# Kernel optimization log

Hardware: AMD Instinct MI355X
Metric: run time of the kernel (lower is better)

Reference implementation:

```python
import jax, jax.numpy as jnp
import numpy as np
from jax import lax

C = 128; HEADS = 16; HD = 8; EPS = 1e-5

def _conv3x3(x, w):
    return lax.conv_general_dilated(x, w, (1, 1), 'SAME', dimension_numbers=('NCHW', 'OIHW', 'NCHW'))

def _cbr3(x, w, g, b):
    # Conv3x3 + BatchNorm(eval, running stats folded -> per-channel affine) + ReLU
    return jax.nn.relu(_conv3x3(x, w) * g[:, None, None] + b[:, None, None])

def _cbr1(x, w, g, b):
    y = jnp.einsum('bchw,oc->bohw', x, w)
    return jax.nn.relu(y * g[:, None, None] + b[:, None, None])

def _ln(t, g, b):
    mu = t.mean(-1, keepdims=True)
    va = ((t - mu) ** 2).mean(-1, keepdims=True)
    return (t - mu) / jnp.sqrt(va + EPS) * g + b

def _gconv1x1(xf, w, b, groups):
    # grouped 1x1 conv on flattened spatial dim: xf [B,Cin,N], w [Cout, Cin//groups]
    B, Cin, N = xf.shape
    Cout = w.shape[0]
    y = jnp.einsum('bgcn,goc->bgon', xf.reshape(B, groups, Cin // groups, N),
                   w.reshape(groups, Cout // groups, Cin // groups))
    return y.reshape(B, Cout, N) + b[:, None]

def _ss_softmax(a):
    # sign * sqrt(|a| + 1e-5) then softmax (GISSA's custom transform)
    a = jnp.sign(a) * jnp.sqrt(jnp.abs(a) + 1e-5)
    return jax.nn.softmax(a, axis=-1)

def _gissa(ximg, qkv_w, qkv_b, g, b, qkv2_w, qkv2_b):
    B, Cc, H, W = ximg.shape
    N = H * W
    xf = ximg.reshape(B, Cc, N)
    qkv = _gconv1x1(xf, qkv_w, qkv_b, HEADS).reshape(B, 3, HEADS, HD, N)
    q, k, v = qkv[:, 0], qkv[:, 1], qkv[:, 2]
    attn = _ss_softmax(jnp.einsum('bhdn,bhen->bhde', q, k) * HD ** -0.5)  # [B,h,hd,hd]
    x1 = jnp.einsum('bhde,bhen->bhdn', attn, v).reshape(B, Cc, N) + xf
    x1 = x1.reshape(B, HEADS, HD, N).transpose(0, 2, 1, 3).reshape(B, Cc, N)  # channel shuffle
    y = x1 * g[:, None] + b[:, None]  # BatchNorm eval affine
    xr = jax.nn.relu(y)
    qkv2 = _gconv1x1(xr, qkv2_w, qkv2_b, HD).reshape(B, 3, HD, HEADS, N)
    q2, k2, v2 = qkv2[:, 0], qkv2[:, 1], qkv2[:, 2]
    attn2 = _ss_softmax(jnp.einsum('bdhn,bdgn->bdhg', q2, k2) * HEADS ** -0.5)  # [B,hd,h,h]
    o = jnp.einsum('bdhg,bdgn->bdhn', attn2, v2).transpose(0, 2, 1, 3).reshape(B, Cc, N) + y
    return o.reshape(B, Cc, H, W)

def _swsa_calc(ximg, pi_w, pi_b, g, b, po_w, po_b):
    B, Cc, H, W = ximg.shape
    t = jnp.einsum('bcn,oc->bon', ximg.reshape(B, Cc, H * W), pi_w) + pi_b[:, None]
    t = t * g[:, None] + b[:, None]  # BN affine
    q = t[:, :Cc].transpose(0, 2, 1)  # [B,N,C]
    v = t[:, Cc:].transpose(0, 2, 1)
    atn = jax.nn.softmax(jnp.einsum('bnc,bmc->bnm', q, q) * Cc ** -0.5, axis=-1)
    y = jnp.einsum('bnm,bmc->bnc', atn, v).transpose(0, 2, 1)  # [B,C,N]
    y = (jnp.einsum('bcn,oc->bon', y, po_w) + po_b[:, None]).reshape(B, Cc, H, W)
    return y, atn

def _swsa_reuse(ximg, atn, pi_w, pi_b, g, b, po_w, po_b):
    B, Cc, H, W = ximg.shape
    t = jnp.einsum('bcn,oc->bon', ximg.reshape(B, Cc, H * W), pi_w) + pi_b[:, None]
    t = t * g[:, None] + b[:, None]
    v = t.transpose(0, 2, 1)
    y = (jnp.einsum('bnm,bmc->bnc', atn, v) * Cc ** -0.5).transpose(0, 2, 1)
    return (jnp.einsum('bcn,oc->bon', y, po_w) + po_b[:, None]).reshape(B, Cc, H, W)

def _forward(x, ssfe_w, ssfe_g, ssfe_b, cc_w, cc_g, cc_b, ln1_g, ln1_b, qkv_w, qkv_b, gbn_g, gbn_b, qkv2_w, qkv2_b, ln2_g, ln2_b, mlp_w1, mlp_b1, mlp_w2, mlp_b2, cs_w, cs_g, cs_b, lfe0_w, lfe0_g, lfe0_b, s0_pi_w, s0_pi_b, s0_bn_g, s0_bn_b, s0_po_w, s0_po_b, lfe1_w, lfe1_g, lfe1_b, s1_pi_w, s1_pi_b, s1_bn_g, s1_bn_b, s1_po_w, s1_po_b, lamuda, fc_w):
    B, Cin, H, W = x.shape
    N = H * W
    # SSFE stem (approximated as Conv3x3+BN+ReLU; source def unavailable)
    xs = _cbr3(x, ssfe_w, ssfe_g, ssfe_b)
    # channel branch: 1x1 CBR + SIT (LN -> GISSA -> residual -> LN -> MLP -> residual)
    xc = _cbr1(xs, cc_w, cc_g, cc_b)
    t = xc.reshape(B, C, N).transpose(0, 2, 1)  # [B,N,C]
    cur = _ln(t, ln1_g, ln1_b).transpose(0, 2, 1).reshape(B, C, H, W)
    t = t + _gissa(cur, qkv_w, qkv_b, gbn_g, gbn_b, qkv2_w, qkv2_b).reshape(B, C, N).transpose(0, 2, 1)
    h = _ln(t, ln2_g, ln2_b)
    h = jax.nn.gelu(h @ mlp_w1.T + mlp_b1, approximate=False) @ mlp_w2.T + mlp_b2
    t = t + h
    xc = t.transpose(0, 2, 1).reshape(B, C, H, W)
    # spatial branch: 3x3 CBR + SCA (LFE + SWSA with attention reuse)
    xp = _cbr3(xs, cs_w, cs_g, cs_b)
    xp = _cbr3(xp, lfe0_w, lfe0_g, lfe0_b) + xp
    y, atn = _swsa_calc(xp, s0_pi_w, s0_pi_b, s0_bn_g, s0_bn_b, s0_po_w, s0_po_b)
    xp = y + xp
    xp = _cbr3(xp, lfe1_w, lfe1_g, lfe1_b) + xp
    xp = _swsa_reuse(xp, atn, s1_pi_w, s1_pi_b, s1_bn_g, s1_bn_b, s1_po_w, s1_po_b) + xp
    lmd = jax.nn.sigmoid(lamuda[0])
    out = lmd * xc + (1.0 - lmd) * xp
    return out.mean(axis=(2, 3)) @ fc_w.T  # global avg pool + fc (dropout p=0 for HUST2013)

def setup_inputs():
    ks = iter(jax.random.split(jax.random.key(0), 64))
    def rn(shape, scale=0.05):
        return jax.random.normal(next(ks), shape, jnp.float32) * scale
    ones = lambda *s: jnp.ones(s, jnp.float32)
    zeros = lambda *s: jnp.zeros(s, jnp.float32)
    return dict(
        x=jax.random.normal(next(ks), (32, 144, 32, 32), jnp.float32),
        ssfe_w=rn((144, 144, 3, 3)), ssfe_g=ones(144), ssfe_b=zeros(144),
        cc_w=rn((128, 144)), cc_g=ones(128), cc_b=zeros(128),
        ln1_g=ones(128), ln1_b=zeros(128),
        qkv_w=rn((384, 8)), qkv_b=zeros(384),
        gbn_g=ones(128), gbn_b=zeros(128),
        qkv2_w=rn((384, 16)), qkv2_b=zeros(384),
        ln2_g=ones(128), ln2_b=zeros(128),
        mlp_w1=rn((512, 128)), mlp_b1=zeros(512),
        mlp_w2=rn((128, 512)), mlp_b2=zeros(128),
        cs_w=rn((128, 144, 3, 3)), cs_g=ones(128), cs_b=zeros(128),
        lfe0_w=rn((128, 128, 3, 3)), lfe0_g=ones(128), lfe0_b=zeros(128),
        s0_pi_w=rn((256, 128)), s0_pi_b=zeros(256), s0_bn_g=ones(256), s0_bn_b=zeros(256),
        s0_po_w=rn((128, 128)), s0_po_b=zeros(128),
        lfe1_w=rn((128, 128, 3, 3)), lfe1_g=ones(128), lfe1_b=zeros(128),
        s1_pi_w=rn((128, 128)), s1_pi_b=zeros(128), s1_bn_g=ones(128), s1_bn_b=zeros(128),
        s1_po_w=rn((128, 128)), s1_po_b=zeros(128),
        lamuda=jnp.full((1,), 0.5, jnp.float32),
        fc_w=rn((16, 128)),
    )

def reference(x, ssfe_w, ssfe_g, ssfe_b, cc_w, cc_g, cc_b, ln1_g, ln1_b, qkv_w, qkv_b, gbn_g, gbn_b, qkv2_w, qkv2_b, ln2_g, ln2_b, mlp_w1, mlp_b1, mlp_w2, mlp_b2, cs_w, cs_g, cs_b, lfe0_w, lfe0_g, lfe0_b, s0_pi_w, s0_pi_b, s0_bn_g, s0_bn_b, s0_po_w, s0_po_b, lfe1_w, lfe1_g, lfe1_b, s1_pi_w, s1_pi_b, s1_bn_g, s1_bn_b, s1_po_w, s1_po_b, lamuda, fc_w):
    return _forward(x, ssfe_w, ssfe_g, ssfe_b, cc_w, cc_g, cc_b, ln1_g, ln1_b, qkv_w, qkv_b, gbn_g, gbn_b, qkv2_w, qkv2_b, ln2_g, ln2_b, mlp_w1, mlp_b1, mlp_w2, mlp_b2, cs_w, cs_g, cs_b, lfe0_w, lfe0_g, lfe0_b, s0_pi_w, s0_pi_b, s0_bn_g, s0_bn_b, s0_po_w, s0_po_b, lfe1_w, lfe1_g, lfe1_b, s1_pi_w, s1_pi_b, s1_bn_g, s1_bn_b, s1_po_w, s1_po_b, lamuda, fc_w)
```

## Files before the change

kernel.cpp:

```cpp
#include <hip/hip_runtime.h>
#include <math.h>


static constexpr int NPIX = 1024;

typedef __attribute__((ext_vector_type(8))) short bf16x8;
typedef __attribute__((ext_vector_type(4))) float f32x4;
typedef __attribute__((ext_vector_type(8))) unsigned short u16x8;
typedef __attribute__((ext_vector_type(4))) unsigned short u16x4;

static __device__ __forceinline__ unsigned short f2bf(float f) {
    unsigned u = __builtin_bit_cast(unsigned, f);
    unsigned r = (u + 0x7fffu + ((u >> 16) & 1u)) >> 16;
    return (unsigned short)r;
}
static __device__ __forceinline__ float bf2f(unsigned short u) {
    unsigned v = ((unsigned)u) << 16;
    return __builtin_bit_cast(float, v);
}

__global__ __launch_bounds__(256) void prepack_convs(
    const float* __restrict__ ssfe_w, const float* __restrict__ cs_w,
    const float* __restrict__ lfe0_w, const float* __restrict__ lfe1_w,
    unsigned short* __restrict__ wssfe, unsigned short* __restrict__ wcs,
    unsigned short* __restrict__ wlfe0, unsigned short* __restrict__ wlfe1)
{
    int idx = blockIdx.x * 256 + threadIdx.x;
    const float* src;
    unsigned short* dst;
    int k, Cout, CIN, CINP;
    if (idx < 207360) {
        src = ssfe_w; dst = wssfe; k = idx; Cout = 144; CIN = 144; CINP = 160;
    } else if (idx < 391680) {
        src = cs_w; dst = wcs; k = idx - 207360; Cout = 128; CIN = 144; CINP = 160;
    } else if (idx < 539136) {
        src = lfe0_w; dst = wlfe0; k = idx - 391680; Cout = 128; CIN = 128; CINP = 128;
    } else if (idx < 686592) {
        src = lfe1_w; dst = wlfe1; k = idx - 539136; Cout = 128; CIN = 128; CINP = 128;
    } else return;
    int ci = k % CINP;
    int rem = k / CINP;
    int co = rem % Cout;
    int tap = rem / Cout;
    float v = (ci < CIN) ? src[((size_t)co * CIN + ci) * 9 + tap] : 0.f;
    dst[k] = f2bf(v);
}

__global__ __launch_bounds__(256) void prepack_lins(
    const float* __restrict__ cc_w, const float* __restrict__ pi0_w,
    const float* __restrict__ pi1_w, const float* __restrict__ po0_w,
    const float* __restrict__ po1_w, const float* __restrict__ w1,
    const float* __restrict__ w2, unsigned short* __restrict__ o)
{
    int idx = blockIdx.x * 256 + threadIdx.x;
    if (idx >= 233472) return;
    float v;
    if (idx < 20480) {
        int ci = idx % 160, co = idx / 160;
        v = (ci < 144) ? cc_w[co * 144 + ci] : 0.f;
    } else if (idx < 53248) {
        v = pi0_w[idx - 20480];
    } else if (idx < 69632) {
        v = pi1_w[idx - 53248];
    } else if (idx < 86016) {
        v = po0_w[idx - 69632];
    } else if (idx < 102400) {
        v = po1_w[idx - 86016];
    } else if (idx < 167936) {
        v = w1[idx - 102400];
    } else {
        v = w2[idx - 167936];
    }
    o[idx] = f2bf(v);
}

__global__ __launch_bounds__(256) void cvt_xT_kernel(
    const float* __restrict__ x, unsigned short* __restrict__ xT0)
{
    __shared__ unsigned short T[64 * 168];
    const int tid = threadIdx.x;
    const int b = blockIdx.x;
    const int px0 = blockIdx.y << 6;
    const float* xb = x + ((size_t)b * 144 << 10) + px0;

#pragma unroll 1
    for (int idx = tid; idx < 72 * 64; idx += 256) {
        const int c2 = idx >> 6, px = idx & 63;
        float a = xb[((size_t)(2 * c2) << 10) + px];
        float c = xb[((size_t)(2 * c2 + 1) << 10) + px];
        *(unsigned*)&T[px * 168 + 2 * c2] =
            (unsigned)f2bf(a) | ((unsigned)f2bf(c) << 16);
    }
#pragma unroll 1
    for (int idx = tid; idx < 64 * 8; idx += 256) {
        const int px = idx >> 3, pr = idx & 7;
        *(unsigned*)&T[px * 168 + 144 + pr * 2] = 0u;
    }
    __syncthreads();

#pragma unroll 1
    for (int idx = tid; idx < 64 * 20; idx += 256) {
        const int px = idx / 20;
        const int chunk = idx - px * 20;
        *(u16x8*)(xT0 + ((size_t)((b << 10) + px0 + px)) * 160 + chunk * 8) =
            *(const u16x8*)&T[px * 168 + chunk * 8];
    }
}

__global__ __launch_bounds__(256) void conv3x3_ssfe_kernel(
    const unsigned short* __restrict__ xT,
    const unsigned short* __restrict__ wrep,
    const float* __restrict__ g, const float* __restrict__ bb,
    unsigned short* __restrict__ outT)
{
    constexpr int CINP = 160, PITCH = 168, NCHK = 20;
    __shared__ unsigned short X[130 * PITCH];
    const int tid = threadIdx.x;
    const int b = blockIdx.x, gr = blockIdx.y;
    const int pbase = gr << 6;
    const int gbase = pbase - 33;
    const int wid = tid >> 6, lane = tid & 63;
    const int ll = lane & 15, lq = lane >> 4;
    const unsigned short* xb = xT + ((size_t)b << 10) * CINP;

#pragma unroll 1
    for (int idx = tid; idx < 130 * NCHK; idx += 256) {
        const int row = idx / NCHK;
        const int chunk = idx - row * NCHK;
        const int gp = gbase + row;
        u16x8 v = {};
        if (gp >= 0 && gp < 1024)
            v = *(const u16x8*)(xb + (size_t)gp * CINP + chunk * 8);
        *(u16x8*)&X[row * PITCH + chunk * 8] = v;
    }
    __syncthreads();

    if (wid == 3) {
#pragma unroll
        for (int j = 0; j < 4; ++j) {
            const int px = pbase + j * 16 + ll;
            u16x4 z = {};
            *(u16x4*)(outT + ((size_t)((b << 10) + px)) * 160 + 144 + lq * 4) = z;
        }
        return;
    }

    const int co0w = wid * 48;
    f32x4 acc[3][4];
#pragma unroll
    for (int i = 0; i < 3; ++i)
#pragma unroll
        for (int j = 0; j < 4; ++j)
#pragma unroll
            for (int r = 0; r < 4; ++r) acc[i][j][r] = 0.f;

#pragma unroll
    for (int tap = 0; tap < 9; ++tap) {
        const int soff = (tap / 3) * 32 + (tap % 3);
        const int dx = tap % 3;
#pragma unroll
        for (int kc = 0; kc < CINP / 32; ++kc) {
            bf16x8 bfv[4];
#pragma unroll
            for (int j = 0; j < 4; ++j) {
                const int p = j * 16 + ll;
                bf16x8 v = *(const bf16x8*)&X[(p + soff) * PITCH + kc * 32 + lq * 8];
                const bool zed = (dx == 0 && (j & 1) == 0 && ll == 0) ||
                                 (dx == 2 && (j & 1) == 1 && ll == 15);
                if (zed) { bf16x8 z = {}; v = z; }
                bfv[j] = v;
            }
            const unsigned short* wb =
                wrep + ((size_t)tap * 144 + co0w) * CINP + kc * 32 + lq * 8;
#pragma unroll
            for (int i = 0; i < 3; ++i) {
                bf16x8 af = *(const bf16x8*)(wb + (size_t)(i * 16 + ll) * CINP);
#pragma unroll
                for (int j = 0; j < 4; ++j)
                    acc[i][j] = __builtin_amdgcn_mfma_f32_16x16x32_bf16(
                        af, bfv[j], acc[i][j], 0, 0, 0);
            }
        }
    }

#pragma unroll
    for (int i = 0; i < 3; ++i) {
        const int cob = co0w + i * 16 + lq * 4;
        float gv[4], bv[4];
#pragma unroll
        for (int r = 0; r < 4; ++r) { gv[r] = g[cob + r]; bv[r] = bb[cob + r]; }
#pragma unroll
        for (int j = 0; j < 4; ++j) {
            const int px = pbase + j * 16 + ll;
            u16x4 tp;
#pragma unroll
            for (int r = 0; r < 4; ++r)
                tp[r] = f2bf(fmaxf(acc[i][j][r] * gv[r] + bv[r], 0.f));
            *(u16x4*)(outT + ((size_t)((b << 10) + px)) * 160 + cob) = tp;
        }
    }
}

template <int CINP>
__global__ __launch_bounds__(256) void conv3x3_lds_kernel(
    const unsigned short* __restrict__ xT,
    const unsigned short* __restrict__ wrep,
    const float* __restrict__ g, const float* __restrict__ bb,
    const unsigned short* __restrict__ resT,
    unsigned short* __restrict__ outT, int Cout)
{
    constexpr int PITCH = CINP + 8;
    constexpr int NCHK = CINP / 8;
    __shared__ unsigned short X[130 * PITCH];
    const int tid = threadIdx.x;
    const int b = blockIdx.x, gr = blockIdx.y;
    const int pbase = gr << 6;
    const int gbase = pbase - 33;
    const int wid = tid >> 6, lane = tid & 63;
    const int ll = lane & 15, lq = lane >> 4;
    const int co0w = wid << 5;
    const unsigned short* xb = xT + ((size_t)b << 10) * CINP;

#pragma unroll 1
    for (int idx = tid; idx < 130 * NCHK; idx += 256) {
        const int row = idx / NCHK;
        const int chunk = idx - row * NCHK;
        const int gp = gbase + row;
        u16x8 v = {};
        if (gp >= 0 && gp < 1024)
            v = *(const u16x8*)(xb + (size_t)gp * CINP + chunk * 8);
        *(u16x8*)&X[row * PITCH + chunk * 8] = v;
    }
    __syncthreads();

    f32x4 acc[2][4];
#pragma unroll
    for (int i = 0; i < 2; ++i)
#pragma unroll
        for (int j = 0; j < 4; ++j)
#pragma unroll
            for (int r = 0; r < 4; ++r) acc[i][j][r] = 0.f;

#pragma unroll
    for (int tap = 0; tap < 9; ++tap) {
        const int soff = (tap / 3) * 32 + (tap % 3);
        const int dx = tap % 3;
#pragma unroll
        for (int kc = 0; kc < CINP / 32; ++kc) {
            bf16x8 bfv[4];
#pragma unroll
            for (int j = 0; j < 4; ++j) {
                const int p = j * 16 + ll;
                bf16x8 v = *(const bf16x8*)&X[(p + soff) * PITCH + kc * 32 + lq * 8];
                const bool zed = (dx == 0 && (j & 1) == 0 && ll == 0) ||
                                 (dx == 2 && (j & 1) == 1 && ll == 15);
                if (zed) { bf16x8 z = {}; v = z; }
                bfv[j] = v;
            }
            const unsigned short* wb =
                wrep + ((size_t)tap * Cout + co0w) * CINP + kc * 32 + lq * 8;
#pragma unroll
            for (int i = 0; i < 2; ++i) {
                bf16x8 af = *(const bf16x8*)(wb + (size_t)(i * 16 + ll) * CINP);
#pragma unroll
                for (int j = 0; j < 4; ++j)
                    acc[i][j] = __builtin_amdgcn_mfma_f32_16x16x32_bf16(
                        af, bfv[j], acc[i][j], 0, 0, 0);
            }
        }
    }

#pragma unroll
    for (int i = 0; i < 2; ++i) {
        const int cob = co0w + i * 16 + lq * 4;
        float gv[4], bv[4];
#pragma unroll
        for (int r = 0; r < 4; ++r) { gv[r] = g[cob + r]; bv[r] = bb[cob + r]; }
#pragma unroll
        for (int j = 0; j < 4; ++j) {
            const int px = pbase + j * 16 + ll;
            const size_t rowT = ((size_t)((b << 10) + px)) << 7;
            u16x4 rv = {};
            if (resT) rv = *(const u16x4*)(resT + rowT + cob);
            u16x4 tp;
#pragma unroll
            for (int r = 0; r < 4; ++r) {
                float v = fmaxf(acc[i][j][r] * gv[r] + bv[r], 0.f);
                if (resT) v += bf2f(rv[r]);
                tp[r] = f2bf(v);
            }
            *(u16x4*)(outT + rowT + cob) = tp;
        }
    }
}

template <int KP>
__global__ __launch_bounds__(256) void lin_mfma_kernel(
    const unsigned short* __restrict__ xT, const unsigned short* __restrict__ wbf,
    const float* __restrict__ bias0, const float* __restrict__ g,
    const float* __restrict__ bb, const unsigned short* __restrict__ resT,
    float* __restrict__ outF, unsigned short* __restrict__ outBF,
    unsigned short* __restrict__ outT, int do_relu)
{
    const int tid = threadIdx.x;
    const int b = blockIdx.x;
    const int n0 = blockIdx.y << 6;
    const int wid = tid >> 6, lane = tid & 63;
    const int ll = lane & 15, lq = lane >> 4;
    const unsigned short* xb = xT + (size_t)((b << 10) + n0) * KP;

    f32x4 acc[2][4];
#pragma unroll
    for (int i = 0; i < 2; ++i)
#pragma unroll
        for (int j = 0; j < 4; ++j)
#pragma unroll
            for (int r = 0; r < 4; ++r) acc[i][j][r] = 0.f;

#pragma unroll
    for (int kk = 0; kk < KP / 32; ++kk) {
        bf16x8 af[2], bfv[4];
#pragma unroll
        for (int i = 0; i < 2; ++i)
            af[i] = *(const bf16x8*)(wbf + (size_t)(wid * 32 + i * 16 + ll) * KP + kk * 32 + lq * 8);
#pragma unroll
        for (int j = 0; j < 4; ++j)
            bfv[j] = *(const bf16x8*)(xb + (size_t)(j * 16 + ll) * KP + kk * 32 + lq * 8);
#pragma unroll
        for (int i = 0; i < 2; ++i)
#pragma unroll
            for (int j = 0; j < 4; ++j)
                acc[i][j] = __builtin_amdgcn_mfma_f32_16x16x32_bf16(af[i], bfv[j], acc[i][j], 0, 0, 0);
    }

#pragma unroll
    for (int i = 0; i < 2; ++i) {
        const int cob = wid * 32 + i * 16 + lq * 4;
        float b0v[4], gv[4], bv[4];
#pragma unroll
        for (int r = 0; r < 4; ++r) {
            b0v[r] = bias0 ? bias0[cob + r] : 0.f;
            gv[r] = g ? g[cob + r] : 1.f;
            bv[r] = g ? bb[cob + r] : 0.f;
        }
#pragma unroll
        for (int j = 0; j < 4; ++j) {
            const int px = n0 + j * 16 + ll;
            const size_t rowT = ((size_t)((b << 10) + px)) << 7;
            u16x4 rv = {};
            if (resT) rv = *(const u16x4*)(resT + rowT + cob);
            u16x4 tp;
#pragma unroll
            for (int r = 0; r < 4; ++r) {
                const int co = cob + r;
                float v = acc[i][j][r] + b0v[r];
                v = v * gv[r] + bv[r];
                if (do_relu) v = fmaxf(v, 0.f);
                if (resT) v += bf2f(rv[r]);
                if (outF) outF[((size_t)((b << 7) + co) << 10) + px] = v;
                unsigned short h = f2bf(v);
                if (outBF) outBF[((size_t)((b << 7) + co) << 10) + px] = h;
                tp[r] = h;
            }
            if (outT) *(u16x4*)(outT + rowT + cob) = tp;
        }
    }
}

__global__ __launch_bounds__(256) void ln_kernel(
    const float* __restrict__ in, const float* __restrict__ g,
    const float* __restrict__ bb, unsigned short* __restrict__ out_bf,
    unsigned short* __restrict__ outT)
{
    const int tid = threadIdx.x;
    const int b = blockIdx.x >> 2;
    const int n = ((blockIdx.x & 3) << 8) + tid;
    const float* ib = in + ((size_t)b << 17) + n;
    float s = 0.f, sq = 0.f;
#pragma unroll 8
    for (int c = 0; c < 128; ++c) {
        float v = ib[(size_t)c << 10];
        s += v;
        sq += v * v;
    }
    const float mu = s * 0.0078125f;
    const float r = rsqrtf(sq * 0.0078125f - mu * mu + 1e-5f);
    unsigned short* obf = out_bf + ((size_t)b << 17) + n;
    unsigned short* oT = outT + (((size_t)b << 10) + n) * 128;
#pragma unroll 2
    for (int c0 = 0; c0 < 128; c0 += 8) {
        u16x8 pk;
#pragma unroll
        for (int e = 0; e < 8; ++e) {
            const int c = c0 + e;
            float v = ib[(size_t)c << 10];
            float y = (v - mu) * r * g[c] + bb[c];
            unsigned short h = f2bf(y);
            obf[(size_t)c << 10] = h;
            pk[e] = h;
        }
        *(u16x8*)(oT + c0) = pk;
    }
}

__global__ __launch_bounds__(256) void gram_kernel(
    const unsigned short* __restrict__ Xbf, float* __restrict__ G)
{
    __shared__ unsigned short Xs[128 * 128];
    const int tid = threadIdx.x;
    const int b = blockIdx.x >> 2;
    const int rg = blockIdx.x & 3;
    const int wid = tid >> 6, lane = tid & 63;
    const int lq = lane >> 4, ll = lane & 15;
    const unsigned short* Xb = Xbf + ((size_t)b << 17);

    f32x4 acc[2][2];
#pragma unroll
    for (int mi = 0; mi < 2; ++mi)
#pragma unroll
        for (int ci = 0; ci < 2; ++ci)
#pragma unroll
            for (int r = 0; r < 4; ++r) acc[mi][ci][r] = 0.f;

#pragma unroll 1
    for (int nt = 0; nt < 8; ++nt) {
        const int n0 = nt << 7;
#pragma unroll
        for (int p = 0; p < 8; ++p) {
            const int ch = (p << 4) + (tid >> 4);
            const int seg = (tid & 15) << 3;
            *(u16x8*)&Xs[ch * 128 + (seg ^ ((ch & 7) << 3))] =
                *(const u16x8*)(Xb + ((size_t)ch << 10) + n0 + seg);
        }
        __syncthreads();
#pragma unroll
        for (int ks = 0; ks < 4; ++ks) {
            bf16x8 af[2], bf_[2];
#pragma unroll
            for (int mi = 0; mi < 2; ++mi) {
                const int ar = (rg << 5) + mi * 16 + ll;
                af[mi] = *(const bf16x8*)&Xs[ar * 128 + ((ks * 32 + lq * 8) ^ ((ar & 7) << 3))];
            }
#pragma unroll
            for (int ci = 0; ci < 2; ++ci) {
                const int br = (wid << 5) + ci * 16 + ll;
                bf_[ci] = *(const bf16x8*)&Xs[br * 128 + ((ks * 32 + lq * 8) ^ ((br & 7) << 3))];
            }
#pragma unroll
            for (int mi = 0; mi < 2; ++mi)
#pragma unroll
                for (int ci = 0; ci < 2; ++ci)
                    acc[mi][ci] = __builtin_amdgcn_mfma_f32_16x16x32_bf16(
                        af[mi], bf_[ci], acc[mi][ci], 0, 0, 0);
        }
        __syncthreads();
    }
    float* Gb = G + ((size_t)b << 14);
#pragma unroll
    for (int mi = 0; mi < 2; ++mi)
#pragma unroll
        for (int ci = 0; ci < 2; ++ci)
#pragma unroll
            for (int r = 0; r < 4; ++r) {
                const int row = (rg << 5) + mi * 16 + lq * 4 + r;
                const int col = (wid << 5) + ci * 16 + ll;
                Gb[row * 128 + col] = acc[mi][ci][r];
            }
}

__global__ __launch_bounds__(256) void sums_kernel(
    const unsigned short* __restrict__ Xbf, float* __restrict__ S)
{
    const int tid = threadIdx.x;
    const int b = blockIdx.x;
    const int ch = tid >> 1, half = tid & 1;
    const unsigned short* p = Xbf + ((size_t)b << 17) + ((size_t)ch << 10) + half * 512;
    float s = 0.f;
#pragma unroll 4
    for (int i = 0; i < 64; ++i) {
        u16x8 v = *(const u16x8*)(p + i * 8);
#pragma unroll
        for (int e = 0; e < 8; ++e) s += bf2f(v[e]);
    }
    s += __shfl_xor(s, 1);
    if (half == 0) S[(b << 7) + ch] = s;
}

__global__ __launch_bounds__(64) void mats1_kernel(
    const float* __restrict__ G, const float* __restrict__ S,
    const float* __restrict__ qkv_w, const float* __restrict__ qkv_b,
    const float* __restrict__ g, const float* __restrict__ bb,
    unsigned short* __restrict__ M1, float* __restrict__ c1)
{
    const int lane = threadIdx.x;
    const int b = blockIdx.x >> 4, h = blockIdx.x & 15;
    const float* Gb = G + ((size_t)b << 14);
    const float* Sb = S + (b << 7);
    const int d = lane >> 3, e = lane & 7;
    const int qch = h * 8 + d, kch = 128 + h * 8 + e;
    const int qoff = (qch / 24) * 8, koff = (kch / 24) * 8;
    float wq[8], wk[8];
#pragma unroll
    for (int i = 0; i < 8; ++i) {
        wq[i] = qkv_w[qch * 8 + i];
        wk[i] = qkv_w[kch * 8 + i];
    }
    float s = 0.f;
#pragma unroll
    for (int i = 0; i < 8; ++i) {
        float gu = 0.f;
#pragma unroll
        for (int j = 0; j < 8; ++j) gu += Gb[(qoff + i) * 128 + koff + j] * wk[j];
        s += wq[i] * gu;
    }
    const float bq = qkv_b[qch], bk = qkv_b[kch];
    float swk = 0.f, swq = 0.f;
#pragma unroll
    for (int j = 0; j < 8; ++j) { swk += wk[j] * Sb[koff + j]; swq += wq[j] * Sb[qoff + j]; }
    s += bq * swk + bk * swq + 1024.f * bq * bk;
    s *= 0.35355339059327373f;
    float a = (s > 0.f) ? sqrtf(s + 1e-5f) : ((s < 0.f) ? -sqrtf(1e-5f - s) : 0.f);
    float mx = a;
    mx = fmaxf(mx, __shfl_xor(mx, 1));
    mx = fmaxf(mx, __shfl_xor(mx, 2));
    mx = fmaxf(mx, __shfl_xor(mx, 4));
    float p = __expf(a - mx);
    float den = p;
    den += __shfl_xor(den, 1);
    den += __shfl_xor(den, 2);
    den += __shfl_xor(den, 4);
    const float A = p / den;

    const int l = e;
    const int cp = d * 16 + h;
    float row[16];
#pragma unroll
    for (int j = 0; j < 16; ++j) row[j] = 0.f;
    float cacc = 0.f;
#pragma unroll
    for (int e2 = 0; e2 < 8; ++e2) {
        const float Ae = __shfl(A, d * 8 + e2);
        const int vch = 256 + h * 8 + e2;
        const int voff = (vch / 24) * 8;
        cacc += Ae * qkv_b[vch];
        if ((voff >> 4) == l) {
            const int base = voff & 15;
#pragma unroll
            for (int j = 0; j < 8; ++j) row[base + j] += Ae * qkv_w[vch * 8 + j];
        }
    }
    const int idc = h * 8 + d;
    if ((idc >> 4) == l) row[idc & 15] += 1.f;
    const float gg = g[cp];
    unsigned short* mrow = M1 + ((size_t)b << 14) + cp * 128 + l * 16;
#pragma unroll
    for (int j = 0; j < 16; ++j) mrow[j] = f2bf(gg * row[j]);
    if (l == 0) c1[(b << 7) + cp] = gg * cacc + bb[cp];
}

__global__ __launch_bounds__(256) void mats2_kernel(
    const float* __restrict__ G, const float* __restrict__ S,
    const float* __restrict__ qkv2_w, const float* __restrict__ qkv2_b,
    unsigned short* __restrict__ M2, float* __restrict__ c2)
{
    const int tid = threadIdx.x;
    const int b = blockIdx.x >> 3, d = blockIdx.x & 7;
    const float* Gb = G + ((size_t)b << 14);
    const float* Sb = S + (b << 7);
    const int h = tid >> 4, gq = tid & 15;
    const int q2ch = d * 16 + h, k2ch = 128 + d * 16 + gq;
    const int qoff = (q2ch / 48) * 16, koff = (k2ch / 48) * 16;
    float wq[16], wk[16];
#pragma unroll
    for (int i = 0; i < 16; ++i) {
        wq[i] = qkv2_w[q2ch * 16 + i];
        wk[i] = qkv2_w[k2ch * 16 + i];
    }
    float s = 0.f;
#pragma unroll
    for (int i = 0; i < 16; ++i) {
        float gu = 0.f;
#pragma unroll
        for (int j = 0; j < 16; ++j) gu += Gb[(qoff + i) * 128 + koff + j] * wk[j];
        s += wq[i] * gu;
    }
    const float bq = qkv2_b[q2ch], bk = qkv2_b[k2ch];
    float swk = 0.f, swq = 0.f;
#pragma unroll
    for (int j = 0; j < 16; ++j) { swk += wk[j] * Sb[koff + j]; swq += wq[j] * Sb[qoff + j]; }
    s += bq * swk + bk * swq + 1024.f * bq * bk;
    s *= 0.25f;
    float a = (s > 0.f) ? sqrtf(s + 1e-5f) : ((s < 0.f) ? -sqrtf(1e-5f - s) : 0.f);
    float mx = a;
    mx = fmaxf(mx, __shfl_xor(mx, 1));
    mx = fmaxf(mx, __shfl_xor(mx, 2));
    mx = fmaxf(mx, __shfl_xor(mx, 4));
    mx = fmaxf(mx, __shfl_xor(mx, 8));
    float p = __expf(a - mx);
    float den = p;
    den += __shfl_xor(den, 1);
    den += __shfl_xor(den, 2);
    den += __shfl_xor(den, 4);
    den += __shfl_xor(den, 8);
    const float A2 = p / den;

    const int l = gq;
    float row[8];
#pragma unroll
    for (int j = 0; j < 8; ++j) row[j] = 0.f;
    float cacc = 0.f;
#pragma unroll
    for (int g2 = 0; g2 < 16; ++g2) {
        const float Ag = __shfl(A2, (tid & 48) + g2);
        const int v2ch = 256 + d * 16 + g2;
        const int voff = (v2ch / 48) * 16;
        cacc += Ag * qkv2_b[v2ch];
        if ((l >> 1) == (voff >> 4)) {
            const int base = (l & 1) * 8;
#pragma unroll
            for (int j = 0; j < 8; ++j) row[j] += Ag * qkv2_w[v2ch * 16 + base + j];
        }
    }
    const int c = h * 8 + d;
    unsigned short* mrow = M2 + ((size_t)b << 14) + c * 128 + l * 8;
#pragma unroll
    for (int j = 0; j < 8; ++j) mrow[j] = f2bf(row[j]);
    if (l == 0) c2[(b << 7) + c] = cacc;
}

__global__ __launch_bounds__(256) void apply1_mfma_kernel(
    const unsigned short* __restrict__ curT, const unsigned short* __restrict__ M1bf,
    const float* __restrict__ c1, float* __restrict__ ybuf,
    unsigned short* __restrict__ yrbf, unsigned short* __restrict__ yrT)
{
    const int tid = threadIdx.x;
    const int b = blockIdx.x >> 3;
    const int n0 = (blockIdx.x & 7) << 7;
    const int wid = tid >> 6, lane = tid & 63;
    const int wr = wid >> 1, wc = wid & 1;
    const int ll = lane & 15, lq = lane >> 4;
    const unsigned short* Mb = M1bf + ((size_t)b << 14);
    const unsigned short* xb = curT + (((size_t)b << 10) + n0 + wc * 64) * 128;

    f32x4 acc[4][4];
#pragma unroll
    for (int i = 0; i < 4; ++i)
#pragma unroll
        for (int j = 0; j < 4; ++j)
#pragma unroll
            for (int r = 0; r < 4; ++r) acc[i][j][r] = 0.f;

#pragma unroll
    for (int kk = 0; kk < 4; ++kk) {
        bf16x8 af[4], bfv[4];
#pragma unroll
        for (int i = 0; i < 4; ++i)
            af[i] = *(const bf16x8*)(Mb + (size_t)(wr * 64 + i * 16 + ll) * 128 + kk * 32 + lq * 8);
#pragma unroll
        for (int j = 0; j < 4; ++j)
            bfv[j] = *(const bf16x8*)(xb + (size_t)(j * 16 + ll) * 128 + kk * 32 + lq * 8);
#pragma unroll
        for (int i = 0; i < 4; ++i)
#pragma unroll
            for (int j = 0; j < 4; ++j)
                acc[i][j] = __builtin_amdgcn_mfma_f32_16x16x32_bf16(af[i], bfv[j], acc[i][j], 0, 0, 0);
    }

#pragma unroll
    for (int i = 0; i < 4; ++i) {
        const int cob = wr * 64 + i * 16 + lq * 4;
        float c1v[4];
#pragma unroll
        for (int r = 0; r < 4; ++r) c1v[r] = c1[(b << 7) + cob + r];
#pragma unroll
        for (int j = 0; j < 4; ++j) {
            const int px = n0 + wc * 64 + j * 16 + ll;
            u16x4 tp;
#pragma unroll
            for (int r = 0; r < 4; ++r) {
                const int co = cob + r;
                const float v = acc[i][j][r] + c1v[r];
                const size_t oi = ((size_t)(b * 128 + co) << 10) + px;
                ybuf[oi] = v;
                const unsigned short h = f2bf(fmaxf(v, 0.f));
                yrbf[oi] = h;
                tp[r] = h;
            }
            *(u16x4*)(yrT + (((size_t)b << 10) + px) * 128 + cob) = tp;
        }
    }
}

__global__ __launch_bounds__(256) void apply2_mfma_kernel(
    const unsigned short* __restrict__ yrT, const unsigned short* __restrict__ M2bf,
    const float* __restrict__ c2, const float* __restrict__ ybuf,
    float* __restrict__ t)
{
    const int tid = threadIdx.x;
    const int b = blockIdx.x >> 3;
    const int n0 = (blockIdx.x & 7) << 7;
    const int wid = tid >> 6, lane = tid & 63;
    const int wr = wid >> 1, wc = wid & 1;
    const int ll = lane & 15, lq = lane >> 4;
    const unsigned short* Mb = M2bf + ((size_t)b << 14);
    const unsigned short* xb = yrT + (((size_t)b << 10) + n0 + wc * 64) * 128;

    f32x4 acc[4][4];
#pragma unroll
    for (int i = 0; i < 4; ++i)
#pragma unroll
        for (int j = 0; j < 4; ++j)
#pragma unroll
            for (int r = 0; r < 4; ++r) acc[i][j][r] = 0.f;

#pragma unroll
    for (int kk = 0; kk < 4; ++kk) {
        bf16x8 af[4], bfv[4];
#pragma unroll
        for (int i = 0; i < 4; ++i)
            af[i] = *(const bf16x8*)(Mb + (size_t)(wr * 64 + i * 16 + ll) * 128 + kk * 32 + lq * 8);
#pragma unroll
        for (int j = 0; j < 4; ++j)
            bfv[j] = *(const bf16x8*)(xb + (size_t)(j * 16 + ll) * 128 + kk * 32 + lq * 8);
#pragma unroll
        for (int i = 0; i < 4; ++i)
#pragma unroll
            for (int j = 0; j < 4; ++j)
                acc[i][j] = __builtin_amdgcn_mfma_f32_16x16x32_bf16(af[i], bfv[j], acc[i][j], 0, 0, 0);
    }

#pragma unroll
    for (int i = 0; i < 4; ++i) {
        const int cob = wr * 64 + i * 16 + lq * 4;
        float c2v[4];
#pragma unroll
        for (int r = 0; r < 4; ++r) c2v[r] = c2[(b << 7) + cob + r];
#pragma unroll
        for (int j = 0; j < 4; ++j) {
            const int px = n0 + wc * 64 + j * 16 + ll;
#pragma unroll
            for (int r = 0; r < 4; ++r) {
                const size_t oi = ((size_t)(b * 128 + cob + r) << 10) + px;
                t[oi] += acc[i][j][r] + c2v[r] + ybuf[oi];
            }
        }
    }
}

__global__ __launch_bounds__(256) void mlp_mfma_kernel(
    float* __restrict__ t, const float* __restrict__ ln_g,
    const float* __restrict__ ln_b, const unsigned short* __restrict__ w1bf,
    const float* __restrict__ b1, const unsigned short* __restrict__ w2bf,
    const float* __restrict__ b2)
{
    __shared__ unsigned char lds[16384 + 65536];
    unsigned char* xnb = lds;
    unsigned char* hb = lds + 16384;

    const int tid = threadIdx.x;
    const int b = blockIdx.x >> 4;
    const int n0 = (blockIdx.x & 15) << 6;
    float* tb = t + ((size_t)b << 17) + n0;

    {
        const int px = tid >> 2, q = tid & 3;
        float v[32];
        float s = 0.f, sq = 0.f;
#pragma unroll
        for (int k = 0; k < 32; ++k) {
            float x = tb[((size_t)(q * 32 + k) << 10) + px];
            v[k] = x;
            s += x;
            sq += x * x;
        }
        s += __shfl_xor(s, 1); s += __shfl_xor(s, 2);
        sq += __shfl_xor(sq, 1); sq += __shfl_xor(sq, 2);
        const float mu = s * 0.0078125f;
        const float rstd = rsqrtf(sq * 0.0078125f - mu * mu + 1e-5f);
        const int sw = (px & 7) << 4;
#pragma unroll
        for (int cc = 0; cc < 4; ++cc) {
            u16x8 pk;
#pragma unroll
            for (int e = 0; e < 8; ++e) {
                int c = q * 32 + cc * 8 + e;
                float xv = (v[cc * 8 + e] - mu) * rstd * ln_g[c] + ln_b[c];
                pk[e] = f2bf(xv);
            }
            *(u16x8*)(xnb + px * 256 + ((q * 64 + cc * 16) ^ sw)) = pk;
        }
    }
    __syncthreads();

    const int wid = tid >> 6, lane = tid & 63;
    const int lr = lane & 15, lk = lane >> 4;

#pragma unroll 1
    for (int pass = 0; pass < 2; ++pass) {
        const int hidbase = (wid << 7) + (pass << 6);
        f32x4 acc[4][4];
#pragma unroll
        for (int i = 0; i < 4; ++i)
#pragma unroll
            for (int j = 0; j < 4; ++j)
#pragma unroll
                for (int r = 0; r < 4; ++r) acc[i][j][r] = 0.f;
#pragma unroll
        for (int kk = 0; kk < 4; ++kk) {
            bf16x8 af[4], bfr[4];
#pragma unroll
            for (int i = 0; i < 4; ++i)
                af[i] = *(const bf16x8*)(w1bf + (size_t)(hidbase + i * 16 + lr) * 128 + kk * 32 + lk * 8);
#pragma unroll
            for (int j = 0; j < 4; ++j) {
                const int px = j * 16 + lr;
                bfr[j] = *(const bf16x8*)(xnb + px * 256 + ((kk * 64 + lk * 16) ^ ((px & 7) << 4)));
            }
#pragma unroll
            for (int i = 0; i < 4; ++i)
#pragma unroll
                for (int j = 0; j < 4; ++j)
                    acc[i][j] = __builtin_amdgcn_mfma_f32_16x16x32_bf16(af[i], bfr[j], acc[i][j], 0, 0, 0);
        }
#pragma unroll
        for (int i = 0; i < 4; ++i) {
            const int hid0 = hidbase + i * 16 + lk * 4;
            float bi[4];
#pragma unroll
            for (int r = 0; r < 4; ++r) bi[r] = b1[hid0 + r];
#pragma unroll
            for (int j = 0; j < 4; ++j) {
                const int px = j * 16 + lr;
                u16x4 pk;
#pragma unroll
                for (int r = 0; r < 4; ++r) {
                    float x = acc[i][j][r] + bi[r];
                    float u = 1.5957691f * x * (1.f + 0.044715f * x * x);
                    float gv = x / (1.f + __expf(-u));
                    pk[r] = f2bf(gv);
                }
                *(u16x4*)(hb + px * 1024 + ((hid0 * 2) ^ ((px & 7) << 4))) = pk;
            }
        }
    }
    __syncthreads();

    f32x4 acc2[2][4];
#pragma unroll
    for (int i = 0; i < 2; ++i)
#pragma unroll
        for (int j = 0; j < 4; ++j)
#pragma unroll
            for (int r = 0; r < 4; ++r) acc2[i][j][r] = 0.f;
#pragma unroll 2
    for (int ks = 0; ks < 16; ++ks) {
        bf16x8 af[2], bfr[4];
#pragma unroll
        for (int i = 0; i < 2; ++i)
            af[i] = *(const bf16x8*)(w2bf + (size_t)((wid << 5) + i * 16 + lr) * 512 + ks * 32 + lk * 8);
#pragma unroll
        for (int j = 0; j < 4; ++j) {
            const int px = j * 16 + lr;
            bfr[j] = *(const bf16x8*)(hb + px * 1024 + ((ks * 64 + lk * 16) ^ ((px & 7) << 4)));
        }
#pragma unroll
        for (int i = 0; i < 2; ++i)
#pragma unroll
            for (int j = 0; j < 4; ++j)
                acc2[i][j] = __builtin_amdgcn_mfma_f32_16x16x32_bf16(af[i], bfr[j], acc2[i][j], 0, 0, 0);
    }
#pragma unroll
    for (int i = 0; i < 2; ++i) {
        const int cb = (wid << 5) + i * 16 + lk * 4;
        float b2v[4];
#pragma unroll
        for (int r = 0; r < 4; ++r) b2v[r] = b2[cb + r];
#pragma unroll
        for (int j = 0; j < 4; ++j) {
            const int px = j * 16 + lr;
#pragma unroll
            for (int r = 0; r < 4; ++r) {
                const size_t off = ((size_t)(cb + r) << 10) + px;
                tb[off] += acc2[i][j][r] + b2v[r];
            }
        }
    }
}

__global__ __launch_bounds__(256) void swsa_mfma_kernel(
    const unsigned short* __restrict__ qT, const unsigned short* __restrict__ vbf,
    float* __restrict__ outp, unsigned short* __restrict__ outT, float fscale)
{
    __shared__ unsigned short K_lds[128 * 128];
    __shared__ unsigned short V_lds[128 * 128];
    const int tid = threadIdx.x;
    const int b = blockIdx.x & 31;
    const int n0 = (blockIdx.x >> 5) << 6;
    const int wid = tid >> 6, lane = tid & 63;
    const int lq = lane >> 4, ll = lane & 15;
    const unsigned short* qTb = qT + ((size_t)b << 17);
    const unsigned short* vb = vbf + ((size_t)b << 17);

    bf16x8 aq[4];
    {
        const int row = n0 + wid * 16 + ll;
#pragma unroll
        for (int kk = 0; kk < 4; ++kk)
            aq[kk] = *(const bf16x8*)(qTb + ((size_t)row << 7) + kk * 32 + lq * 8);
    }

    float mrun[4], lrun[4];
#pragma unroll
    for (int i = 0; i < 4; ++i) { mrun[i] = -INFINITY; lrun[i] = 0.f; }
    f32x4 yacc[8];
#pragma unroll
    for (int cj = 0; cj < 8; ++cj)
#pragma unroll
        for (int r = 0; r < 4; ++r) yacc[cj][r] = 0.f;

#pragma unroll 1
    for (int mt = 0; mt < 8; ++mt) {
        const int m0 = mt << 7;
        for (int ch = tid; ch < 2048; ch += 256) {
            const int rr = ch >> 4, e0 = (ch & 15) << 3;
            const int sw = (rr & 7) << 3;
            *(u16x8*)&K_lds[rr * 128 + (e0 ^ sw)] =
                *(const u16x8*)(qTb + ((size_t)(m0 + rr) << 7) + e0);
            *(u16x8*)&V_lds[rr * 128 + (e0 ^ sw)] =
                *(const u16x8*)(vb + ((size_t)rr << 10) + m0 + e0);
        }
        __syncthreads();

        f32x4 sacc[8];
#pragma unroll
        for (int j = 0; j < 8; ++j)
#pragma unroll
            for (int r = 0; r < 4; ++r) sacc[j][r] = 0.f;
#pragma unroll
        for (int j = 0; j < 8; ++j) {
            const int ml = j * 16 + ll;
            const int swk = (ml & 7) << 3;
#pragma unroll
            for (int kk = 0; kk < 4; ++kk) {
                bf16x8 bk = *(const bf16x8*)&K_lds[ml * 128 + ((kk * 32 + lq * 8) ^ swk)];
                sacc[j] = __builtin_amdgcn_mfma_f32_16x16x32_bf16(aq[kk], bk, sacc[j], 0, 0, 0);
            }
        }
        __syncthreads();

        float pmax[4];
#pragma unroll
        for (int i = 0; i < 4; ++i) pmax[i] = -INFINITY;
#pragma unroll
        for (int j = 0; j < 8; ++j)
#pragma unroll
            for (int r = 0; r < 4; ++r) {
                float s = sacc[j][r] * 0.08838834764831845f;
                sacc[j][r] = s;
                pmax[r] = fmaxf(pmax[r], s);
            }
        float alpha[4];
#pragma unroll
        for (int i = 0; i < 4; ++i) {
            float m = pmax[i];
            m = fmaxf(m, __shfl_xor(m, 1));
            m = fmaxf(m, __shfl_xor(m, 2));
            m = fmaxf(m, __shfl_xor(m, 4));
            m = fmaxf(m, __shfl_xor(m, 8));
            const float mn = fmaxf(mrun[i], m);
            alpha[i] = __expf(mrun[i] - mn);
            mrun[i] = mn;
        }
        float psum[4];
#pragma unroll
        for (int r = 0; r < 4; ++r) {
            const int nbw = wid * 16 + lq * 4 + r;
            const int sw4 = ((nbw >> 2) & 3) << 4;
            const float mn = mrun[r];
            float ps = 0.f;
#pragma unroll
            for (int j = 0; j < 8; ++j) {
                float p = __expf(sacc[j][r] - mn);
                ps += p;
                K_lds[nbw * 128 + ((j * 16 + ll) ^ sw4)] = f2bf(p);
            }
            psum[r] = ps;
        }
#pragma unroll
        for (int i = 0; i < 4; ++i) {
            float s = psum[i];
            s += __shfl_xor(s, 1);
            s += __shfl_xor(s, 2);
            s += __shfl_xor(s, 4);
            s += __shfl_xor(s, 8);
            lrun[i] = lrun[i] * alpha[i] + s;
        }
#pragma unroll
        for (int cj = 0; cj < 8; ++cj)
#pragma unroll
            for (int r = 0; r < 4; ++r) yacc[cj][r] *= alpha[r];

        bf16x8 ap[4];
        {
            const int nb = wid * 16 + ll;
            const int sw4 = ((nb >> 2) & 3) << 4;
#pragma unroll
            for (int mk = 0; mk < 4; ++mk)
                ap[mk] = *(const bf16x8*)&K_lds[nb * 128 + ((mk * 32 + lq * 8) ^ sw4)];
        }
#pragma unroll
        for (int cj = 0; cj < 8; ++cj) {
            const int cl = cj * 16 + ll;
            const int sw = (cl & 7) << 3;
#pragma unroll
            for (int mk = 0; mk < 4; ++mk) {
                bf16x8 bv = *(const bf16x8*)&V_lds[cl * 128 + ((mk * 32 + lq * 8) ^ sw)];
                yacc[cj] = __builtin_amdgcn_mfma_f32_16x16x32_bf16(ap[mk], bv, yacc[cj], 0, 0, 0);
            }
        }
        __syncthreads();
    }

    const int nbase = n0 + wid * 16 + lq * 4;
    float inv[4];
#pragma unroll
    for (int r = 0; r < 4; ++r) inv[r] = fscale / lrun[r];
#pragma unroll
    for (int cj = 0; cj < 8; ++cj) {
        const int c = cj * 16 + ll;
        float4 o;
        o.x = yacc[cj][0] * inv[0];
        o.y = yacc[cj][1] * inv[1];
        o.z = yacc[cj][2] * inv[2];
        o.w = yacc[cj][3] * inv[3];
        if (outp)
            *(float4*)(outp + ((size_t)(b * 128 + c) << 10) + nbase) = o;
        if (outT) {
            unsigned short* tb = outT + ((size_t)((b << 10) + nbase)) * 128 + c;
            tb[0] = f2bf(o.x);
            tb[128] = f2bf(o.y);
            tb[256] = f2bf(o.z);
            tb[384] = f2bf(o.w);
        }
    }
}

__global__ __launch_bounds__(256) void mean_kernel(
    const float* __restrict__ xc, const float* __restrict__ xp,
    const float* __restrict__ lamuda, float* __restrict__ meanb)
{
    const int wid = threadIdx.x >> 6, lane = threadIdx.x & 63;
    const int row = (blockIdx.x << 2) + wid;
    const float lmd = 1.f / (1.f + __expf(-lamuda[0]));
    const float* a = xc + ((size_t)row << 10) + (lane << 2);
    const float* d = xp + ((size_t)row << 10) + (lane << 2);
    float s = 0.f;
#pragma unroll
    for (int i = 0; i < 4; ++i) {
        float4 va = *(const float4*)(a + (i << 8));
        float4 vd = *(const float4*)(d + (i << 8));
        s += lmd * (va.x + va.y + va.z + va.w) +
             (1.f - lmd) * (vd.x + vd.y + vd.z + vd.w);
    }
#pragma unroll
    for (int o = 1; o < 64; o <<= 1) s += __shfl_xor(s, o);
    if (lane == 0) meanb[row] = s * (1.f / 1024.f);
}

__global__ __launch_bounds__(256) void fc_kernel(
    const float* __restrict__ meanb, const float* __restrict__ fc_w,
    float* __restrict__ outp)
{
    const int idx = blockIdx.x * 256 + threadIdx.x;
    if (idx >= 512) return;
    const int b = idx >> 4, o = idx & 15;
    float s = 0.f;
#pragma unroll 4
    for (int c = 0; c < 128; ++c) s += fc_w[o * 128 + c] * meanb[b * 128 + c];
    outp[b * 16 + o] = s;
}

extern "C" void kernel_launch(void* const* d_in, const int* in_sizes, int n_in,
                              void* d_out, int out_size, void* d_ws, size_t ws_size,
                              hipStream_t stream)
{
    (void)in_sizes; (void)n_in; (void)out_size; (void)ws_size;

    const float* x       = (const float*)d_in[0];
    const float* ssfe_w  = (const float*)d_in[1];
    const float* ssfe_g  = (const float*)d_in[2];
    const float* ssfe_b  = (const float*)d_in[3];
    const float* cc_w    = (const float*)d_in[4];
    const float* cc_g    = (const float*)d_in[5];
    const float* cc_b    = (const float*)d_in[6];
    const float* ln1_g   = (const float*)d_in[7];
    const float* ln1_b   = (const float*)d_in[8];
    const float* qkv_w   = (const float*)d_in[9];
    const float* qkv_b   = (const float*)d_in[10];
    const float* gbn_g   = (const float*)d_in[11];
    const float* gbn_b   = (const float*)d_in[12];
    const float* qkv2_w  = (const float*)d_in[13];
    const float* qkv2_b  = (const float*)d_in[14];
    const float* ln2_g   = (const float*)d_in[15];
    const float* ln2_b   = (const float*)d_in[16];
    const float* mlp_w1  = (const float*)d_in[17];
    const float* mlp_b1  = (const float*)d_in[18];
    const float* mlp_w2  = (const float*)d_in[19];
    const float* mlp_b2  = (const float*)d_in[20];
    const float* cs_w    = (const float*)d_in[21];
    const float* cs_g    = (const float*)d_in[22];
    const float* cs_b    = (const float*)d_in[23];
    const float* lfe0_w  = (const float*)d_in[24];
    const float* lfe0_g  = (const float*)d_in[25];
    const float* lfe0_b  = (const float*)d_in[26];
    const float* s0_pi_w = (const float*)d_in[27];
    const float* s0_pi_b = (const float*)d_in[28];
    const float* s0_bn_g = (const float*)d_in[29];
    const float* s0_bn_b = (const float*)d_in[30];
    const float* s0_po_w = (const float*)d_in[31];
    const float* s0_po_b = (const float*)d_in[32];
    const float* lfe1_w  = (const float*)d_in[33];
    const float* lfe1_g  = (const float*)d_in[34];
    const float* lfe1_b  = (const float*)d_in[35];
    const float* s1_pi_w = (const float*)d_in[36];
    const float* s1_pi_b = (const float*)d_in[37];
    const float* s1_bn_g = (const float*)d_in[38];
    const float* s1_bn_b = (const float*)d_in[39];
    const float* s1_po_w = (const float*)d_in[40];
    const float* s1_po_b = (const float*)d_in[41];
    const float* lamuda  = (const float*)d_in[42];
    const float* fc_w    = (const float*)d_in[43];
    float* out = (float*)d_out;
    float* ws = (float*)d_ws;

    float* xs = ws;
    float* t  = ws + 4718592;
    float* P1 = ws + 8912896;
    float* Qr = ws + 13107200;
    float* P2 = ws + 25690112;
    float* P3 = ws + 29884416;
    (void)P1;

    unsigned short* xT0 = (unsigned short*)Qr;

    unsigned short* curbf = (unsigned short*)Qr;
    unsigned short* curT  = (unsigned short*)(Qr + 2097152);
    unsigned short* yrbf  = (unsigned short*)(Qr + 4194304);
    unsigned short* yrT   = (unsigned short*)(Qr + 6291456);
    unsigned short* xsT   = (unsigned short*)(Qr + 8388608);
    float* ybuf = P2;

    unsigned short* xpT   = (unsigned short*)Qr;
    unsigned short* qT0   = (unsigned short*)Qr;
    unsigned short* v0    = (unsigned short*)(Qr + 2097152);
    unsigned short* yvT   = (unsigned short*)(Qr + 4194304);
    unsigned short* v1    = (unsigned short*)(Qr + 4194304);
    unsigned short* xp3T  = (unsigned short*)(Qr + 6291456);
    unsigned short* yv2T  = (unsigned short*)(Qr + 6291456);
    unsigned short* xp2T  = (unsigned short*)(Qr + 8388608);
    unsigned short* xp4T  = (unsigned short*)(Qr + 8388608);

    unsigned short* linw  = (unsigned short*)(Qr + 11010048);
    unsigned short* wcc   = linw;
    unsigned short* wpi0  = linw + 20480;
    unsigned short* wpi1  = linw + 53248;
    unsigned short* wpo0  = linw + 69632;
    unsigned short* wpo1  = linw + 86016;
    unsigned short* w1bf  = linw + 102400;
    unsigned short* w2bf  = linw + 167936;
    float* meanb = Qr + 11200000;

    float* Gbuf  = P3 + 1048576;
    float* Sbuf  = P3 + 1572864;
    unsigned short* M1bf = (unsigned short*)(P3 + 1576960);
    float* c1buf = P3 + 1839104;
    unsigned short* M2bf = (unsigned short*)(P3 + 1843200);
    float* c2buf = P3 + 2105344;

    unsigned short* wssfe = (unsigned short*)P3;
    unsigned short* wcs   = (unsigned short*)(P3 + 131072);
    unsigned short* wlfe0 = (unsigned short*)(P3 + 262144);
    unsigned short* wlfe1 = (unsigned short*)xs;

    const dim3 blk(256);

    prepack_convs<<<dim3((686592 + 255) / 256), blk, 0, stream>>>(
        ssfe_w, cs_w, lfe0_w, lfe1_w, wssfe, wcs, wlfe0, wlfe1);
    prepack_lins<<<dim3((233472 + 255) / 256), blk, 0, stream>>>(
        cc_w, s0_pi_w, s1_pi_w, s0_po_w, s1_po_w, mlp_w1, mlp_w2, linw);

    cvt_xT_kernel<<<dim3(32, 16), blk, 0, stream>>>(x, xT0);
    conv3x3_ssfe_kernel<<<dim3(32, 16), blk, 0, stream>>>(
        xT0, wssfe, ssfe_g, ssfe_b, xsT);
    lin_mfma_kernel<160><<<dim3(32, 16), blk, 0, stream>>>(
        xsT, wcc, nullptr, cc_g, cc_b, nullptr, t, nullptr, nullptr, 1);

    ln_kernel<<<dim3(128), blk, 0, stream>>>(t, ln1_g, ln1_b, curbf, curT);
    gram_kernel<<<dim3(128), blk, 0, stream>>>(curbf, Gbuf);
    sums_kernel<<<dim3(32), blk, 0, stream>>>(curbf, Sbuf);
    mats1_kernel<<<dim3(512), dim3(64), 0, stream>>>(Gbuf, Sbuf, qkv_w, qkv_b, gbn_g, gbn_b, M1bf, c1buf);
    apply1_mfma_kernel<<<dim3(256), blk, 0, stream>>>(curT, M1bf, c1buf, ybuf, yrbf, yrT);
    gram_kernel<<<dim3(128), blk, 0, stream>>>(yrbf, Gbuf);
    sums_kernel<<<dim3(32), blk, 0, stream>>>(yrbf, Sbuf);
    mats2_kernel<<<dim3(256), blk, 0, stream>>>(Gbuf, Sbuf, qkv2_w, qkv2_b, M2bf, c2buf);
    apply2_mfma_kernel<<<dim3(256), blk, 0, stream>>>(yrT, M2bf, c2buf, ybuf, t);

    mlp_mfma_kernel<<<dim3(512), blk, 0, stream>>>(t, ln2_g, ln2_b, w1bf, mlp_b1, w2bf, mlp_b2);

    conv3x3_lds_kernel<160><<<dim3(32, 16), blk, 0, stream>>>(
        xsT, wcs, cs_g, cs_b, nullptr, xpT, 128);
    conv3x3_lds_kernel<128><<<dim3(32, 16), blk, 0, stream>>>(
        xpT, wlfe0, lfe0_g, lfe0_b, xpT, xp2T, 128);
    lin_mfma_kernel<128><<<dim3(32, 16), blk, 0, stream>>>(
        xp2T, wpi0, s0_pi_b, s0_bn_g, s0_bn_b, nullptr, nullptr, nullptr, qT0, 0);
    lin_mfma_kernel<128><<<dim3(32, 16), blk, 0, stream>>>(
        xp2T, wpi0 + (size_t)128 * 128, s0_pi_b + 128, s0_bn_g + 128, s0_bn_b + 128,
        nullptr, nullptr, v0, nullptr, 0);
    swsa_mfma_kernel<<<dim3(512), blk, 0, stream>>>(qT0, v0, nullptr, yvT, 1.0f);
    lin_mfma_kernel<128><<<dim3(32, 16), blk, 0, stream>>>(
        yvT, wpo0, s0_po_b, nullptr, nullptr, xp2T, nullptr, nullptr, xp3T, 0);
    conv3x3_lds_kernel<128><<<dim3(32, 16), blk, 0, stream>>>(
        xp3T, wlfe1, lfe1_g, lfe1_b, xp3T, xp4T, 128);
    lin_mfma_kernel<128><<<dim3(32, 16), blk, 0, stream>>>(
        xp4T, wpi1, s1_pi_b, s1_bn_g, s1_bn_b, nullptr, nullptr, v1, nullptr, 0);
    swsa_mfma_kernel<<<dim3(512), blk, 0, stream>>>(qT0, v1, nullptr, yv2T, 0.08838834764831845f);
    lin_mfma_kernel<128><<<dim3(32, 16), blk, 0, stream>>>(
        yv2T, wpo1, s1_po_b, nullptr, nullptr, xp4T, P3, nullptr, nullptr, 0);

    mean_kernel<<<dim3(1024), blk, 0, stream>>>(t, P3, lamuda, meanb);
    fc_kernel<<<dim3(2), blk, 0, stream>>>(meanb, fc_w, out);
}
```

Before: 449.4 us.

## Read K/V directly from global in SWSA attention, shrink LDS to per-wave P

The SWSA flash-attention kernel no longer stages 128x128 K and V tiles in shared memory each iteration. It reads MFMA operands straight from global memory and keeps only a small per-wave LDS buffer for the softmax probabilities. This removes the block-wide barriers and cuts LDS use from 64KB to 16KB, which should allow more resident blocks. In exchange, every wave re-reads K and V from global/L2, so the block's K/V loads become redundant across its four waves. The unused fp32 output path is also dropped.

```diff
diff --git a/kernel.cpp b/kernel.cpp
--- a/kernel.cpp
+++ b/kernel.cpp
@@ -889,10 +889,9 @@
 
 __global__ __launch_bounds__(256) void swsa_mfma_kernel(
     const unsigned short* __restrict__ qT, const unsigned short* __restrict__ vbf,
-    float* __restrict__ outp, unsigned short* __restrict__ outT, float fscale)
-{
-    __shared__ unsigned short K_lds[128 * 128];
-    __shared__ unsigned short V_lds[128 * 128];
+    unsigned short* __restrict__ outT, float fscale)
+{
+    __shared__ unsigned short P_lds[4 * 16 * 128];
     const int tid = threadIdx.x;
     const int b = blockIdx.x & 31;
     const int n0 = (blockIdx.x >> 5) << 6;
@@ -900,6 +899,7 @@
     const int lq = lane >> 4, ll = lane & 15;
     const unsigned short* qTb = qT + ((size_t)b << 17);
     const unsigned short* vb = vbf + ((size_t)b << 17);
+    unsigned short* Pw = &P_lds[wid * 16 * 128];
 
     bf16x8 aq[4];
     {
@@ -921,15 +921,6 @@
 #pragma unroll 1
     for (int mt = 0; mt < 8; ++mt) {
         const int m0 = mt << 7;
-        for (int ch = tid; ch < 2048; ch += 256) {
-            const int rr = ch >> 4, e0 = (ch & 15) << 3;
-            const int sw = (rr & 7) << 3;
-            *(u16x8*)&K_lds[rr * 128 + (e0 ^ sw)] =
-                *(const u16x8*)(qTb + ((size_t)(m0 + rr) << 7) + e0);
-            *(u16x8*)&V_lds[rr * 128 + (e0 ^ sw)] =
-                *(const u16x8*)(vb + ((size_t)rr << 10) + m0 + e0);
-        }
-        __syncthreads();
 
         f32x4 sacc[8];
 #pragma unroll
@@ -938,15 +929,13 @@
             for (int r = 0; r < 4; ++r) sacc[j][r] = 0.f;
 #pragma unroll
         for (int j = 0; j < 8; ++j) {
-            const int ml = j * 16 + ll;
-            const int swk = (ml & 7) << 3;
+            const int ml = m0 + j * 16 + ll;
 #pragma unroll
             for (int kk = 0; kk < 4; ++kk) {
-                bf16x8 bk = *(const bf16x8*)&K_lds[ml * 128 + ((kk * 32 + lq * 8) ^ swk)];
+                bf16x8 bk = *(const bf16x8*)(qTb + ((size_t)ml << 7) + kk * 32 + lq * 8);
                 sacc[j] = __builtin_amdgcn_mfma_f32_16x16x32_bf16(aq[kk], bk, sacc[j], 0, 0, 0);
             }
         }
-        __syncthreads();
 
         float pmax[4];
 #pragma unroll
@@ -974,15 +963,15 @@
         float psum[4];
 #pragma unroll
         for (int r = 0; r < 4; ++r) {
-            const int nbw = wid * 16 + lq * 4 + r;
-            const int sw4 = ((nbw >> 2) & 3) << 4;
+            const int rw = lq * 4 + r;
+            const int sw4 = ((rw >> 2) & 3) << 4;
             const float mn = mrun[r];
             float ps = 0.f;
 #pragma unroll
             for (int j = 0; j < 8; ++j) {
                 float p = __expf(sacc[j][r] - mn);
                 ps += p;
-                K_lds[nbw * 128 + ((j * 16 + ll) ^ sw4)] = f2bf(p);
+                Pw[rw * 128 + ((j * 16 + ll) ^ sw4)] = f2bf(p);
             }
             psum[r] = ps;
         }
@@ -1002,23 +991,20 @@
 
         bf16x8 ap[4];
         {
-            const int nb = wid * 16 + ll;
-            const int sw4 = ((nb >> 2) & 3) << 4;
+            const int sw4 = ((ll >> 2) & 3) << 4;
 #pragma unroll
             for (int mk = 0; mk < 4; ++mk)
-                ap[mk] = *(const bf16x8*)&K_lds[nb * 128 + ((mk * 32 + lq * 8) ^ sw4)];
+                ap[mk] = *(const bf16x8*)&Pw[ll * 128 + ((mk * 32 + lq * 8) ^ sw4)];
         }
 #pragma unroll
         for (int cj = 0; cj < 8; ++cj) {
-            const int cl = cj * 16 + ll;
-            const int sw = (cl & 7) << 3;
+            const int c = cj * 16 + ll;
 #pragma unroll
             for (int mk = 0; mk < 4; ++mk) {
-                bf16x8 bv = *(const bf16x8*)&V_lds[cl * 128 + ((mk * 32 + lq * 8) ^ sw)];
+                bf16x8 bv = *(const bf16x8*)(vb + ((size_t)c << 10) + m0 + mk * 32 + lq * 8);
                 yacc[cj] = __builtin_amdgcn_mfma_f32_16x16x32_bf16(ap[mk], bv, yacc[cj], 0, 0, 0);
             }
         }
-        __syncthreads();
     }
 
     const int nbase = n0 + wid * 16 + lq * 4;
@@ -1028,20 +1014,11 @@
 #pragma unroll
     for (int cj = 0; cj < 8; ++cj) {
         const int c = cj * 16 + ll;
-        float4 o;
-        o.x = yacc[cj][0] * inv[0];
-        o.y = yacc[cj][1] * inv[1];
-        o.z = yacc[cj][2] * inv[2];
-        o.w = yacc[cj][3] * inv[3];
-        if (outp)
-            *(float4*)(outp + ((size_t)(b * 128 + c) << 10) + nbase) = o;
-        if (outT) {
-            unsigned short* tb = outT + ((size_t)((b << 10) + nbase)) * 128 + c;
-            tb[0] = f2bf(o.x);
-            tb[128] = f2bf(o.y);
-            tb[256] = f2bf(o.z);
-            tb[384] = f2bf(o.w);
-        }
+        unsigned short* tb = outT + ((size_t)((b << 10) + nbase)) * 128 + c;
+        tb[0]   = f2bf(yacc[cj][0] * inv[0]);
+        tb[128] = f2bf(yacc[cj][1] * inv[1]);
+        tb[256] = f2bf(yacc[cj][2] * inv[2]);
+        tb[384] = f2bf(yacc[cj][3] * inv[3]);
     }
 }
 
@@ -1135,11 +1112,9 @@
 
     float* xs = ws;
     float* t  = ws + 4718592;
-    float* P1 = ws + 8912896;
     float* Qr = ws + 13107200;
     float* P2 = ws + 25690112;
     float* P3 = ws + 29884416;
-    (void)P1;
 
     unsigned short* xT0 = (unsigned short*)Qr;
 
@@ -1216,14 +1191,14 @@
     lin_mfma_kernel<128><<<dim3(32, 16), blk, 0, stream>>>(
         xp2T, wpi0 + (size_t)128 * 128, s0_pi_b + 128, s0_bn_g + 128, s0_bn_b + 128,
         nullptr, nullptr, v0, nullptr, 0);
-    swsa_mfma_kernel<<<dim3(512), blk, 0, stream>>>(qT0, v0, nullptr, yvT, 1.0f);
+    swsa_mfma_kernel<<<dim3(512), blk, 0, stream>>>(qT0, v0, yvT, 1.0f);
     lin_mfma_kernel<128><<<dim3(32, 16), blk, 0, stream>>>(
         yvT, wpo0, s0_po_b, nullptr, nullptr, xp2T, nullptr, nullptr, xp3T, 0);
     conv3x3_lds_kernel<128><<<dim3(32, 16), blk, 0, stream>>>(
         xp3T, wlfe1, lfe1_g, lfe1_b, xp3T, xp4T, 128);
     lin_mfma_kernel<128><<<dim3(32, 16), blk, 0, stream>>>(
         xp4T, wpi1, s1_pi_b, s1_bn_g, s1_bn_b, nullptr, nullptr, v1, nullptr, 0);
-    swsa_mfma_kernel<<<dim3(512), blk, 0, stream>>>(qT0, v1, nullptr, yv2T, 0.08838834764831845f);
+    swsa_mfma_kernel<<<dim3(512), blk, 0, stream>>>(qT0, v1, yv2T, 0.08838834764831845f);
     lin_mfma_kernel<128><<<dim3(32, 16), blk, 0, stream>>>(
         yv2T, wpo1, s1_po_b, nullptr, nullptr, xp4T, P3, nullptr, nullptr, 0);
 
```

Result: slower. 595.7 us (+32.6%).
